# Performance work log

Hardware: AMD Instinct MI355X
Metric: run time of the kernel (lower is better)

Reference implementation:

```python
import jax, jax.numpy as jnp
import numpy as np

B, T, C, H = 4, 2048, 1024, 16
INIT_STD = 0.02

def setup_inputs() -> dict:
    key = jax.random.key(0)
    ks = jax.random.split(key, 9)
    x = jax.random.normal(ks[0], (B, T, C), dtype=jnp.float32)
    def dense(kw):
        return jax.random.normal(kw, (C, C), dtype=jnp.float32) * INIT_STD
    return {
        "x": x,
        "Wq": dense(ks[1]), "bq": jnp.zeros((C,), jnp.float32),
        "Wk": dense(ks[2]), "bk": jnp.zeros((C,), jnp.float32),
        "Wv": dense(ks[3]), "bv": jnp.zeros((C,), jnp.float32),
        "Wo": dense(ks[4]), "bo": jnp.zeros((C,), jnp.float32),
    }

def reference(x, Wq, bq, Wk, bk, Wv, bv, Wo, bo):
    b, t, c = x.shape
    hd = c // H  # head dim
    # QKV projections, reshape to (B, H, T, hd)
    def split_heads(y):
        return jnp.transpose(y.reshape(b, t, H, hd), (0, 2, 1, 3))
    q = split_heads(x @ Wq + bq)
    k = split_heads(x @ Wk + bk)
    v = split_heads(x @ Wv + bv)
    scale = 1.0 / jnp.sqrt(jnp.float32(hd))
    att = jnp.einsum('bhqd,bhkd->bhqk', q, k) * scale  # [B,H,T,T]
    mask = jnp.tril(jnp.ones((t, t), dtype=bool))[None, None]
    att = jnp.where(mask, att, jnp.float32(-jnp.inf))
    att = jax.nn.softmax(att, axis=-1)
    y = jnp.einsum('bhqk,bhkd->bhqd', att, v)  # [B,H,T,hd]
    y = jnp.transpose(y, (0, 2, 1, 3)).reshape(b, t, c)
    return y @ Wo + bo
```

## Files before the change

### kernel.cpp

```cpp
#include <hip/hip_runtime.h>
#include <hip/hip_bf16.h>
#include <stdint.h>

typedef __bf16 bf16;
typedef __attribute__((ext_vector_type(8))) __bf16 bf16x8;
typedef __attribute__((ext_vector_type(4))) __bf16 bf16x4;
typedef __attribute__((ext_vector_type(4))) float f32x4;

constexpr int Bn = 4, Tn = 2048, Cn = 1024, Hn = 16, HD = 64;
constexpr int Mn = Bn * Tn;

__device__ __forceinline__ void gl_lds16(const void* g, void* l) {
  __builtin_amdgcn_global_load_lds(
      (const __attribute__((address_space(1))) void*)g,
      (__attribute__((address_space(3))) void*)l, 16u, 0, 0u);
}

__global__ __launch_bounds__(256) void k_cvt_x(const float* __restrict__ x,
                                               bf16* __restrict__ xb) {
  int i = (blockIdx.x * 256 + threadIdx.x) * 8;
  float4 a = *(const float4*)(x + i);
  float4 b = *(const float4*)(x + i + 4);
  bf16x8 v;
  v[0] = (bf16)a.x; v[1] = (bf16)a.y; v[2] = (bf16)a.z; v[3] = (bf16)a.w;
  v[4] = (bf16)b.x; v[5] = (bf16)b.y; v[6] = (bf16)b.z; v[7] = (bf16)b.w;
  *(bf16x8*)(xb + i) = v;
}

__global__ __launch_bounds__(256) void k_tw(const float* __restrict__ W0,
                                            const float* __restrict__ W1,
                                            const float* __restrict__ W2,
                                            const float* __restrict__ W3,
                                            bf16* __restrict__ WT) {
  __shared__ float tile[32][33];
  const float* W = (blockIdx.z == 0) ? W0 : (blockIdx.z == 1) ? W1
                  : (blockIdx.z == 2) ? W2 : W3;
  bf16* out = WT + (size_t)blockIdx.z * Cn * Cn;
  int tx = threadIdx.x & 31, ty = threadIdx.x >> 5;
  int gx = blockIdx.x * 32 + tx;
  int gy = blockIdx.y * 32;
#pragma unroll
  for (int j = 0; j < 32; j += 8)
    tile[ty + j][tx] = W[(size_t)(gy + ty + j) * Cn + gx];
  __syncthreads();
  int ox = blockIdx.y * 32 + tx;
  int oy = blockIdx.x * 32;
#pragma unroll
  for (int j = 0; j < 32; j += 8)
    out[(size_t)(oy + ty + j) * Cn + ox] = (bf16)tile[tx][ty + j];
}

__global__ __launch_bounds__(512, 2) void k_gemm_qkv8(
    const bf16* __restrict__ A, const bf16* __restrict__ BT,
    const float* __restrict__ bq, const float* __restrict__ bk,
    const float* __restrict__ bv, bf16* __restrict__ out, float qscale) {
  __shared__ __align__(16) char sm[131072];
  const int t = threadIdx.x, w = t >> 6, l = t & 63;
  const int g = l >> 4, q16 = l & 15;
  const int wm = w >> 2, wn = w & 3;
  const int b = blockIdx.x;
  const int k8 = b & 7, idx = b >> 3;
  const int n0 = ((k8 & 3) * 3 + idx % 3) * 256;
  const int m0 = (idx / 3 + (k8 >> 2) * 16) * 256;

  const int xm = (q16 & 7) << 4;
  const int qkB0 = q16 * 128 + ((g * 16) ^ xm);
  const int qkB1 = q16 * 128 + ((64 + g * 16) ^ xm);
  const int aB = wm * 16384;
  const int bB = 32768 + (wn >> 1) * 16384 + (wn & 1) * 8192;

  const int row0 = t >> 3;
  const int row1 = row0 + 64;
  const int seg = (t & 7) ^ (row0 & 7);
  const bf16* aS0 = A + (size_t)(m0 + row0) * 1024 + seg * 8;
  const bf16* aS1 = A + (size_t)(m0 + row1) * 1024 + seg * 8;
  const bf16* bS0 = BT + (size_t)(n0 + row0) * 1024 + seg * 8;
  const bf16* bS1 = BT + (size_t)(n0 + row1) * 1024 + seg * 8;

  f32x4 acc[8][4] = {};

#define QSTG_A(NB, H, J)                                                  \
  gl_lds16(aS0 + (H) * 131072 + (J) * 64, sm + (NB) + (H) * 16384 + w * 1024); \
  gl_lds16(aS1 + (H) * 131072 + (J) * 64,                                 \
           sm + (NB) + (H) * 16384 + 8192 + w * 1024);
#define QSTG_B(NB, H, J)                                                  \
  gl_lds16(bS0 + (H) * 131072 + (J) * 64,                                 \
           sm + (NB) + 32768 + (H) * 16384 + w * 1024);                   \
  gl_lds16(bS1 + (H) * 131072 + (J) * 64,                                 \
           sm + (NB) + 32768 + (H) * 16384 + 8192 + w * 1024);
#define QRD_A(DST, BANK, MI)                                              \
  DST[0] = *(const bf16x8*)(sm + (BANK) + aB + (MI) * 2048 + qkB0);       \
  DST[1] = *(const bf16x8*)(sm + (BANK) + aB + (MI) * 2048 + qkB1);
#define QMFMA(AF, MI)                                                     \
  _Pragma("unroll") for (int ni = 0; ni < 4; ++ni) {                      \
    acc[MI][ni] = __builtin_amdgcn_mfma_f32_16x16x32_bf16(                \
        AF[0], bfr[ni][0], acc[MI][ni], 0, 0, 0);                         \
    acc[MI][ni] = __builtin_amdgcn_mfma_f32_16x16x32_bf16(                \
        AF[1], bfr[ni][1], acc[MI][ni], 0, 0, 0);                         \
  }

  QSTG_A(0, 0, 0); QSTG_A(0, 1, 0); QSTG_B(0, 0, 0); QSTG_B(0, 1, 0);

#pragma unroll
  for (int j = 0; j < 16; ++j) {
    const int BANK = (j & 1) ? 65536 : 0;
    const int NB = (j & 1) ? 0 : 65536;
    const bool more = j < 15;
    if (more) { QSTG_A(NB, 0, j + 1); }
    if (more) asm volatile("s_waitcnt vmcnt(2)" ::: "memory");
    else      asm volatile("s_waitcnt vmcnt(0)" ::: "memory");
    __builtin_amdgcn_sched_barrier(0);
    __builtin_amdgcn_s_barrier();
    __builtin_amdgcn_sched_barrier(0);
    bf16x8 bfr[4][2];
#pragma unroll
    for (int ni = 0; ni < 4; ++ni) {
      bfr[ni][0] = *(const bf16x8*)(sm + BANK + bB + ni * 2048 + qkB0);
      bfr[ni][1] = *(const bf16x8*)(sm + BANK + bB + ni * 2048 + qkB1);
    }
    bf16x8 a0[2], a1[2], a2[2], a3[2];
    QRD_A(a0, BANK, 0); QRD_A(a1, BANK, 1);
    __builtin_amdgcn_s_setprio(1);
    QMFMA(a0, 0); QMFMA(a1, 1);
    __builtin_amdgcn_s_setprio(0);
    __builtin_amdgcn_s_barrier();
    if (more) { QSTG_A(NB, 1, j + 1); }
    QRD_A(a2, BANK, 2); QRD_A(a3, BANK, 3);
    __builtin_amdgcn_s_setprio(1);
    QMFMA(a2, 2); QMFMA(a3, 3);
    __builtin_amdgcn_s_setprio(0);
    __builtin_amdgcn_s_barrier();
    if (more) { QSTG_B(NB, 0, j + 1); }
    QRD_A(a0, BANK, 4); QRD_A(a1, BANK, 5);
    __builtin_amdgcn_s_setprio(1);
    QMFMA(a0, 4); QMFMA(a1, 5);
    __builtin_amdgcn_s_setprio(0);
    __builtin_amdgcn_s_barrier();
    if (more) { QSTG_B(NB, 1, j + 1); }
    QRD_A(a2, BANK, 6); QRD_A(a3, BANK, 7);
    __builtin_amdgcn_s_setprio(1);
    QMFMA(a2, 6); QMFMA(a3, 7);
    __builtin_amdgcn_s_setprio(0);
    __builtin_amdgcn_s_barrier();
  }
#undef QSTG_A
#undef QSTG_B
#undef QRD_A
#undef QMFMA

#pragma unroll
  for (int ni = 0; ni < 4; ++ni) {
    int colBase = n0 + wn * 64 + ni * 16;
    int which = colBase >> 10;
    const float* bp = (which == 0) ? bq : (which == 1) ? bk : bv;
    float scl = (which == 0) ? qscale : 1.0f;
    float bval = bp[(colBase & 1023) + q16];
    int hh = (colBase >> 6) & 15;
    int dd = (colBase & 63) + q16;
    size_t obase = (size_t)which * 8388608 + (size_t)hh * (Tn * HD) + dd;
#pragma unroll
    for (int mi = 0; mi < 8; ++mi) {
#pragma unroll
      for (int r = 0; r < 4; ++r) {
        int row = m0 + wm * 128 + mi * 16 + g * 4 + r;
        int bb = row >> 11, tt = row & 2047;
        out[obase + ((size_t)bb * Hn * Tn + tt) * HD] =
            (bf16)((acc[mi][ni][r] + bval) * scl);
      }
    }
  }
}

__global__ __launch_bounds__(256) void k_gemm_o(const bf16* __restrict__ A,
                                                const bf16* __restrict__ BT,
                                                const float* __restrict__ bias,
                                                float* __restrict__ out) {
  constexpr int KD = 1024;
  __shared__ __align__(16) bf16 As[128 * 64];
  __shared__ __align__(16) bf16 Bs[128 * 64];
  const int t = threadIdx.x;
  const int w = t >> 6, l = t & 63;
  const int b = blockIdx.x;
  const int m0 = (b >> 3) * 128, n0 = (b & 7) * 128;
  const int wr = (w >> 1) * 64, wc = (w & 1) * 64;
  f32x4 acc[4][4] = {};

  for (int kt = 0; kt < KD; kt += 64) {
    __syncthreads();
#pragma unroll
    for (int i = 0; i < 4; ++i) {
      int c = i * 256 + t;
      int row = c >> 3;
      int seg = (c & 7) ^ (row & 7);
      gl_lds16(A + (size_t)(m0 + row) * KD + kt + seg * 8,
               (char*)As + i * 4096 + w * 1024);
      gl_lds16(BT + (size_t)(n0 + row) * KD + kt + seg * 8,
               (char*)Bs + i * 4096 + w * 1024);
    }
    __syncthreads();
#pragma unroll
    for (int kc = 0; kc < 2; ++kc) {
      bf16x8 af[4], bg[4];
#pragma unroll
      for (int mi = 0; mi < 4; ++mi) {
        int row = wr + mi * 16 + (l & 15);
        int off = (row * 128 + kc * 64 + (l >> 4) * 16) ^ ((row & 7) << 4);
        af[mi] = *(const bf16x8*)((const char*)As + off);
      }
#pragma unroll
      for (int ni = 0; ni < 4; ++ni) {
        int row = wc + ni * 16 + (l & 15);
        int off = (row * 128 + kc * 64 + (l >> 4) * 16) ^ ((row & 7) << 4);
        bg[ni] = *(const bf16x8*)((const char*)Bs + off);
      }
#pragma unroll
      for (int mi = 0; mi < 4; ++mi)
#pragma unroll
        for (int ni = 0; ni < 4; ++ni)
          acc[mi][ni] = __builtin_amdgcn_mfma_f32_16x16x32_bf16(
              af[mi], bg[ni], acc[mi][ni], 0, 0, 0);
    }
  }
#pragma unroll
  for (int ni = 0; ni < 4; ++ni) {
    int col = n0 + wc + ni * 16 + (l & 15);
    float bv = bias[col];
#pragma unroll
    for (int mi = 0; mi < 4; ++mi) {
#pragma unroll
      for (int r = 0; r < 4; ++r) {
        int row = m0 + wr + mi * 16 + (l >> 4) * 4 + r;
        out[(size_t)row * Cn + col] = acc[mi][ni][r] + bv;
      }
    }
  }
}

__global__ __launch_bounds__(512, 4) void k_attn(const bf16* __restrict__ Q,
                                                 const bf16* __restrict__ K,
                                                 const bf16* __restrict__ V,
                                                 bf16* __restrict__ Y) {
  __shared__ __align__(16) char smem[32768];
  const int t = threadIdx.x, w = t >> 6, l = t & 63;
  const int g = l >> 4, q16 = l & 15;
  const int wg = blockIdx.x;
  const int bh = wg & 63;
  const int qtile = 15 - (wg >> 6);
  const size_t base = (size_t)bh * Tn * HD;
  const bf16* Qh = Q + base;
  const bf16* Vh = V + base;
  const int qg = qtile * 128 + w * 16 + q16;

  bf16x8 aq[2];
#pragma unroll
  for (int kc = 0; kc < 2; ++kc)
    aq[kc] = *(const bf16x8*)(Qh + (size_t)qg * HD + kc * 32 + g * 8);

  const int xm = (q16 & 7) << 4;
  const int qkB0 = q16 * 128 + ((g * 16) ^ xm);
  const int qkB1 = q16 * 128 + ((64 + g * 16) ^ xm);
  const int innerL = (l >> 5) * 64 + ((l & 15) >> 2) * 16 +
                     (((l >> 4) & 1) * 4 + (l & 3)) * 2;
  int stb[8];
#pragma unroll
  for (int j = 0; j < 8; ++j)
    stb[j] = w * 1024 + j * 128 + (innerL ^ (j << 4));

  const int krow = w * 8 + (l >> 3);
  const int kseg = (l & 7) ^ (krow & 7);
  const bf16* kP = K + base + (size_t)krow * HD + kseg * 8;
  const bf16* vP = Vh + (size_t)l * HD + w * 8;

  f32x4 yacc[4] = {};
  float m_ = -1e30f, l_ = 0.f;
  const int nt = 2 * qtile + 2;
  const int it_mask = 2 * qtile + (w >= 4 ? 1 : 0);
  const int diag = (w & 3) * 16 + q16;

#define STAGE_K(KBUF)                           \
  {                                             \
    gl_lds16(kP, smem + (KBUF) + w * 1024);     \
    kP += 4096;                                 \
  }
#define WRITE_V(VBUF, a0)                               \
  {                                                     \
    _Pragma("unroll") for (int j = 0; j < 8; ++j)       \
      *(bf16*)(smem + (VBUF) + stb[j]) = a0[j];         \
  }
#define COMPUTE(KBUF, VBUF, DOMASK)                                          \
  {                                                                          \
    f32x4 s[4] = {};                                                         \
    __builtin_amdgcn_s_setprio(1);                                           \
    _Pragma("unroll") for (int nj = 0; nj < 4; ++nj) {                       \
      bf16x8 ak0 = *(const bf16x8*)(smem + (KBUF) + qkB0 + nj * 2048);       \
      s[nj] = __builtin_amdgcn_mfma_f32_16x16x32_bf16(ak0, aq[0], s[nj], 0, 0, 0); \
      bf16x8 ak1 = *(const bf16x8*)(smem + (KBUF) + qkB1 + nj * 2048);       \
      s[nj] = __builtin_amdgcn_mfma_f32_16x16x32_bf16(ak1, aq[1], s[nj], 0, 0, 0); \
    }                                                                        \
    __builtin_amdgcn_s_setprio(0);                                           \
    if (DOMASK) {                                                            \
      _Pragma("unroll") for (int nj = 0; nj < 4; ++nj)                       \
        _Pragma("unroll") for (int r = 0; r < 4; ++r)                        \
          if (nj * 16 + g * 4 + r > diag) s[nj][r] = -1e30f;                 \
    }                                                                        \
    float mx = fmaxf(fmaxf(fmaxf(s[0][0], s[0][1]), fmaxf(s[0][2], s[0][3])),\
                     fmaxf(fmaxf(s[1][0], s[1][1]), fmaxf(s[1][2], s[1][3])));\
    mx = fmaxf(mx, fmaxf(fmaxf(fmaxf(s[2][0], s[2][1]), fmaxf(s[2][2], s[2][3])),\
                         fmaxf(fmaxf(s[3][0], s[3][1]), fmaxf(s[3][2], s[3][3]))));\
    mx = fmaxf(mx, __shfl_xor(mx, 16));                                      \
    mx = fmaxf(mx, __shfl_xor(mx, 32));                                      \
    float mn = fmaxf(m_, mx);                                                \
    float fac = __builtin_amdgcn_exp2f(m_ - mn);                             \
    m_ = mn;                                                                 \
    float rs = 0.f;                                                          \
    _Pragma("unroll") for (int nj = 0; nj < 4; ++nj)                         \
      _Pragma("unroll") for (int r = 0; r < 4; ++r) {                        \
        float pv = __builtin_amdgcn_exp2f(s[nj][r] - mn);                    \
        s[nj][r] = pv;                                                       \
        rs += pv;                                                            \
      }                                                                      \
    rs += __shfl_xor(rs, 16);                                                \
    rs += __shfl_xor(rs, 32);                                                \
    l_ = l_ * fac + rs;                                                      \
    _Pragma("unroll") for (int ni = 0; ni < 4; ++ni)                         \
      _Pragma("unroll") for (int r = 0; r < 4; ++r) yacc[ni][r] *= fac;      \
    __builtin_amdgcn_s_setprio(1);                                           \
    _Pragma("unroll") for (int vkc = 0; vkc < 2; ++vkc) {                    \
      bf16x8 pb;                                                             \
      _Pragma("unroll") for (int j = 0; j < 4; ++j) {                        \
        pb[j] = (bf16)s[2 * vkc][j];                                         \
        pb[4 + j] = (bf16)s[2 * vkc + 1][j];                                 \
      }                                                                      \
      int vb = (vkc == 0) ? qkB0 : qkB1;                                     \
      _Pragma("unroll") for (int ni = 0; ni < 4; ++ni) {                     \
        bf16x8 va = *(const bf16x8*)(smem + (VBUF) + vb + ni * 2048);        \
        yacc[ni] = __builtin_amdgcn_mfma_f32_16x16x32_bf16(va, pb, yacc[ni], 0, 0, 0); \
      }                                                                      \
    }                                                                        \
    __builtin_amdgcn_s_setprio(0);                                           \
  }

  STAGE_K(0);
  {
    bf16x8 a0 = *(const bf16x8*)vP;
    vP += 4096;
    WRITE_V(16384, a0);
  }

  int it = 0;
  for (;;) {
    __syncthreads();
    bool more = (it + 1) < nt;
    bf16x8 a0;
    if (more) {
      STAGE_K(8192);
      a0 = *(const bf16x8*)vP;
      vP += 4096;
    }
    if (it <= it_mask) COMPUTE(0, 16384, it == it_mask);
    if (more) WRITE_V(24576, a0);
    if (++it >= nt) break;

    __syncthreads();
    more = (it + 1) < nt;
    if (more) {
      STAGE_K(0);
      a0 = *(const bf16x8*)vP;
      vP += 4096;
    }
    if (it <= it_mask) COMPUTE(8192, 24576, it == it_mask);
    if (more) WRITE_V(16384, a0);
    if (++it >= nt) break;
  }
#undef STAGE_K
#undef WRITE_V
#undef COMPUTE

  const int hh = bh & 15, bb = bh >> 4;
  float inv = 1.f / l_;
#pragma unroll
  for (int ni = 0; ni < 4; ++ni) {
    bf16x4 o;
#pragma unroll
    for (int r = 0; r < 4; ++r) o[r] = (bf16)(yacc[ni][r] * inv);
    int d0 = ni * 16 + g * 4;
    *(bf16x4*)&Y[(size_t)(bb * Tn + qg) * Cn + hh * HD + d0] = o;
  }
}

extern "C" void kernel_launch(void* const* d_in, const int* in_sizes, int n_in,
                              void* d_out, int out_size, void* d_ws,
                              size_t ws_size, hipStream_t stream) {
  const float* x  = (const float*)d_in[0];
  const float* Wq = (const float*)d_in[1];
  const float* bq = (const float*)d_in[2];
  const float* Wk = (const float*)d_in[3];
  const float* bk = (const float*)d_in[4];
  const float* Wv = (const float*)d_in[5];
  const float* bv = (const float*)d_in[6];
  const float* Wo = (const float*)d_in[7];
  const float* bo = (const float*)d_in[8];
  char* ws = (char*)d_ws;
  bf16* xb = (bf16*)ws;
  bf16* WT = (bf16*)(ws + (size_t)(16 << 20));
  bf16* Qh = (bf16*)(ws + (size_t)(24 << 20));
  bf16* Kh = (bf16*)(ws + (size_t)(40 << 20));
  bf16* Vh = (bf16*)(ws + (size_t)(56 << 20));
  float* out = (float*)d_out;

  const float QSCALE = 0.125f * 1.44269504088896f;

  k_cvt_x<<<4096, 256, 0, stream>>>(x, xb);
  k_tw<<<dim3(32, 32, 4), 256, 0, stream>>>(Wq, Wk, Wv, Wo, WT);
  k_gemm_qkv8<<<384, 512, 0, stream>>>(xb, WT, bq, bk, bv, Qh, QSCALE);
  k_attn<<<1024, 512, 0, stream>>>(Qh, Kh, Vh, xb);
  k_gemm_o<<<512, 256, 0, stream>>>(xb, WT + (3u << 20), bo, out);
}
```

Before: 158.3 us.

## Shrink QKV GEMM tile to 128x256 and double grid to 768 blocks

The fused QKV projection GEMM moves from 256x256 output tiles (384 blocks) to 128x256 tiles (768 blocks), which halves the per-wave accumulator and cuts LDS from 128KB to 96KB. The staging and barrier schedule is restructured: A and the first half of B are prefetched first, the second half of B is issued midway, and there are now two sub-phases per K step instead of four. It also drops the XCD-aware block swizzle in favour of a plain row-major block mapping. The aim is better CU fill (768 blocks versus 384 on 256 CUs) and lower register pressure, at the cost of lower arithmetic intensity per tile and more global reads of the weight matrix.

```diff
diff --git a/kernel.cpp b/kernel.cpp
--- a/kernel.cpp
+++ b/kernel.cpp
@@ -54,99 +54,84 @@
     const bf16* __restrict__ A, const bf16* __restrict__ BT,
     const float* __restrict__ bq, const float* __restrict__ bk,
     const float* __restrict__ bv, bf16* __restrict__ out, float qscale) {
-  __shared__ __align__(16) char sm[131072];
+  __shared__ __align__(16) char sm[98304];
   const int t = threadIdx.x, w = t >> 6, l = t & 63;
   const int g = l >> 4, q16 = l & 15;
   const int wm = w >> 2, wn = w & 3;
   const int b = blockIdx.x;
-  const int k8 = b & 7, idx = b >> 3;
-  const int n0 = ((k8 & 3) * 3 + idx % 3) * 256;
-  const int m0 = (idx / 3 + (k8 >> 2) * 16) * 256;
+  const int m0 = (b / 12) * 128, n0 = (b % 12) * 256;
 
   const int xm = (q16 & 7) << 4;
   const int qkB0 = q16 * 128 + ((g * 16) ^ xm);
   const int qkB1 = q16 * 128 + ((64 + g * 16) ^ xm);
-  const int aB = wm * 16384;
-  const int bB = 32768 + (wn >> 1) * 16384 + (wn & 1) * 8192;
-
-  const int row0 = t >> 3;
-  const int row1 = row0 + 64;
-  const int seg = (t & 7) ^ (row0 & 7);
-  const bf16* aS0 = A + (size_t)(m0 + row0) * 1024 + seg * 8;
-  const bf16* aS1 = A + (size_t)(m0 + row1) * 1024 + seg * 8;
-  const bf16* bS0 = BT + (size_t)(n0 + row0) * 1024 + seg * 8;
-  const bf16* bS1 = BT + (size_t)(n0 + row1) * 1024 + seg * 8;
-
-  f32x4 acc[8][4] = {};
-
-#define QSTG_A(NB, H, J)                                                  \
-  gl_lds16(aS0 + (H) * 131072 + (J) * 64, sm + (NB) + (H) * 16384 + w * 1024); \
-  gl_lds16(aS1 + (H) * 131072 + (J) * 64,                                 \
-           sm + (NB) + (H) * 16384 + 8192 + w * 1024);
-#define QSTG_B(NB, H, J)                                                  \
-  gl_lds16(bS0 + (H) * 131072 + (J) * 64,                                 \
-           sm + (NB) + 32768 + (H) * 16384 + w * 1024);                   \
-  gl_lds16(bS1 + (H) * 131072 + (J) * 64,                                 \
-           sm + (NB) + 32768 + (H) * 16384 + 8192 + w * 1024);
-#define QRD_A(DST, BANK, MI)                                              \
-  DST[0] = *(const bf16x8*)(sm + (BANK) + aB + (MI) * 2048 + qkB0);       \
-  DST[1] = *(const bf16x8*)(sm + (BANK) + aB + (MI) * 2048 + qkB1);
-#define QMFMA(AF, MI)                                                     \
-  _Pragma("unroll") for (int ni = 0; ni < 4; ++ni) {                      \
-    acc[MI][ni] = __builtin_amdgcn_mfma_f32_16x16x32_bf16(                \
-        AF[0], bfr[ni][0], acc[MI][ni], 0, 0, 0);                         \
-    acc[MI][ni] = __builtin_amdgcn_mfma_f32_16x16x32_bf16(                \
-        AF[1], bfr[ni][1], acc[MI][ni], 0, 0, 0);                         \
-  }
-
-  QSTG_A(0, 0, 0); QSTG_A(0, 1, 0); QSTG_B(0, 0, 0); QSTG_B(0, 1, 0);
+
+  const int srow = t >> 3;
+  const int sseg = (t & 7) ^ (srow & 7);
+  const bf16* aP0 = A + (size_t)(m0 + srow) * 1024 + sseg * 8;
+  const bf16* aP1 = aP0 + 65536;
+  const bf16* bP0 = BT + (size_t)(n0 + srow) * 1024 + sseg * 8;
+  const bf16* bP1 = bP0 + 65536;
+  const bf16* bP2 = bP0 + 131072;
+  const bf16* bP3 = bP0 + 196608;
+
+  f32x4 acc[4][4] = {};
+
+#define STG_A(BK_, J)                                        \
+  gl_lds16(aP0 + (J) * 64, sm + (BK_) + w * 1024);           \
+  gl_lds16(aP1 + (J) * 64, sm + (BK_) + 8192 + w * 1024);
+#define STG_B0(BK_, J)                                       \
+  gl_lds16(bP0 + (J) * 64, sm + (BK_) + 16384 + w * 1024);   \
+  gl_lds16(bP1 + (J) * 64, sm + (BK_) + 24576 + w * 1024);
+#define STG_B1(BK_, J)                                       \
+  gl_lds16(bP2 + (J) * 64, sm + (BK_) + 32768 + w * 1024);   \
+  gl_lds16(bP3 + (J) * 64, sm + (BK_) + 40960 + w * 1024);
+#define RD_A(DST, BK_, MI)                                                  \
+  DST[0] = *(const bf16x8*)(sm + (BK_) + wm * 8192 + (MI) * 2048 + qkB0);   \
+  DST[1] = *(const bf16x8*)(sm + (BK_) + wm * 8192 + (MI) * 2048 + qkB1);
+#define RD_B(DST, BK_, NI)                                                  \
+  DST[0] = *(const bf16x8*)(sm + (BK_) + 16384 + wn * 8192 + (NI) * 2048 + qkB0); \
+  DST[1] = *(const bf16x8*)(sm + (BK_) + 16384 + wn * 8192 + (NI) * 2048 + qkB1);
+#define MFMA_MI(MI, AF)                                                     \
+  _Pragma("unroll") for (int ni = 0; ni < 4; ++ni) {                        \
+    acc[MI][ni] = __builtin_amdgcn_mfma_f32_16x16x32_bf16(                  \
+        AF[0], bfr[ni][0], acc[MI][ni], 0, 0, 0);                           \
+    acc[MI][ni] = __builtin_amdgcn_mfma_f32_16x16x32_bf16(                  \
+        AF[1], bfr[ni][1], acc[MI][ni], 0, 0, 0);                           \
+  }
+
+  STG_A(0, 0); STG_B0(0, 0); STG_B1(0, 0);
 
 #pragma unroll
   for (int j = 0; j < 16; ++j) {
-    const int BANK = (j & 1) ? 65536 : 0;
-    const int NB = (j & 1) ? 0 : 65536;
+    const int BK_ = (j & 1) ? 49152 : 0;
+    const int NB_ = 49152 - BK_;
     const bool more = j < 15;
-    if (more) { QSTG_A(NB, 0, j + 1); }
-    if (more) asm volatile("s_waitcnt vmcnt(2)" ::: "memory");
+    if (more) { STG_A(NB_, j + 1); STG_B0(NB_, j + 1); }
+    if (more) asm volatile("s_waitcnt vmcnt(4)" ::: "memory");
     else      asm volatile("s_waitcnt vmcnt(0)" ::: "memory");
     __builtin_amdgcn_sched_barrier(0);
     __builtin_amdgcn_s_barrier();
-    __builtin_amdgcn_sched_barrier(0);
     bf16x8 bfr[4][2];
-#pragma unroll
-    for (int ni = 0; ni < 4; ++ni) {
-      bfr[ni][0] = *(const bf16x8*)(sm + BANK + bB + ni * 2048 + qkB0);
-      bfr[ni][1] = *(const bf16x8*)(sm + BANK + bB + ni * 2048 + qkB1);
-    }
-    bf16x8 a0[2], a1[2], a2[2], a3[2];
-    QRD_A(a0, BANK, 0); QRD_A(a1, BANK, 1);
+    RD_B(bfr[0], BK_, 0); RD_B(bfr[1], BK_, 1);
+    RD_B(bfr[2], BK_, 2); RD_B(bfr[3], BK_, 3);
+    bf16x8 af0[2], af1[2];
+    RD_A(af0, BK_, 0); RD_A(af1, BK_, 1);
     __builtin_amdgcn_s_setprio(1);
-    QMFMA(a0, 0); QMFMA(a1, 1);
+    MFMA_MI(0, af0); MFMA_MI(1, af1);
+    __builtin_amdgcn_s_setprio(0);
+    if (more) { STG_B1(NB_, j + 1); }
+    RD_A(af0, BK_, 2); RD_A(af1, BK_, 3);
+    __builtin_amdgcn_s_setprio(1);
+    MFMA_MI(2, af0); MFMA_MI(3, af1);
     __builtin_amdgcn_s_setprio(0);
     __builtin_amdgcn_s_barrier();
-    if (more) { QSTG_A(NB, 1, j + 1); }
-    QRD_A(a2, BANK, 2); QRD_A(a3, BANK, 3);
-    __builtin_amdgcn_s_setprio(1);
-    QMFMA(a2, 2); QMFMA(a3, 3);
-    __builtin_amdgcn_s_setprio(0);
-    __builtin_amdgcn_s_barrier();
-    if (more) { QSTG_B(NB, 0, j + 1); }
-    QRD_A(a0, BANK, 4); QRD_A(a1, BANK, 5);
-    __builtin_amdgcn_s_setprio(1);
-    QMFMA(a0, 4); QMFMA(a1, 5);
-    __builtin_amdgcn_s_setprio(0);
-    __builtin_amdgcn_s_barrier();
-    if (more) { QSTG_B(NB, 1, j + 1); }
-    QRD_A(a2, BANK, 6); QRD_A(a3, BANK, 7);
-    __builtin_amdgcn_s_setprio(1);
-    QMFMA(a2, 6); QMFMA(a3, 7);
-    __builtin_amdgcn_s_setprio(0);
-    __builtin_amdgcn_s_barrier();
-  }
-#undef QSTG_A
-#undef QSTG_B
-#undef QRD_A
-#undef QMFMA
+  }
+#undef STG_A
+#undef STG_B0
+#undef STG_B1
+#undef RD_A
+#undef RD_B
+#undef MFMA_MI
 
 #pragma unroll
   for (int ni = 0; ni < 4; ++ni) {
@@ -159,10 +144,10 @@
     int dd = (colBase & 63) + q16;
     size_t obase = (size_t)which * 8388608 + (size_t)hh * (Tn * HD) + dd;
 #pragma unroll
-    for (int mi = 0; mi < 8; ++mi) {
+    for (int mi = 0; mi < 4; ++mi) {
 #pragma unroll
       for (int r = 0; r < 4; ++r) {
-        int row = m0 + wm * 128 + mi * 16 + g * 4 + r;
+        int row = m0 + wm * 64 + mi * 16 + g * 4 + r;
         int bb = row >> 11, tt = row & 2047;
         out[obase + ((size_t)bb * Hn * Tn + tt) * HD] =
             (bf16)((acc[mi][ni][r] + bval) * scl);
@@ -412,7 +397,7 @@
 
   k_cvt_x<<<4096, 256, 0, stream>>>(x, xb);
   k_tw<<<dim3(32, 32, 4), 256, 0, stream>>>(Wq, Wk, Wv, Wo, WT);
-  k_gemm_qkv8<<<384, 512, 0, stream>>>(xb, WT, bq, bk, bv, Qh, QSCALE);
+  k_gemm_qkv8<<<768, 512, 0, stream>>>(xb, WT, bq, bk, bv, Qh, QSCALE);
   k_attn<<<1024, 512, 0, stream>>>(Qh, Kh, Vh, xb);
   k_gemm_o<<<512, 256, 0, stream>>>(xb, WT + (3u << 20), bo, out);
 }
```

Measured after the change: 155.7 us. About the same (-1.6%).
